# Performance work log

Hardware: AMD Instinct MI355X
Metric: run time of the kernel (lower is better)

Reference implementation:

```python
import jax, jax.numpy as jnp
import numpy as np

V, E, HD, K = 100000, 128, 256, 9
B, T = 128, 512
H = HD // 2  # per-direction hidden size


def setup_inputs() -> dict:
    key = jax.random.key(0)
    ks = jax.random.split(key, 16)
    s = 0.1
    rn = lambda k, shape: jax.random.normal(k, shape, jnp.float32) * s
    sentences = jax.random.randint(ks[0], (B, T), 0, V, dtype=jnp.int32)
    lengths = jax.random.randint(ks[1], (B,), 1, T + 1, dtype=jnp.int32)
    return {
        'sentences': sentences,
        'lengths': lengths,
        'embed': rn(ks[2], (V, E)),
        'Wih_f': rn(ks[3], (4 * H, E)), 'Whh_f': rn(ks[4], (4 * H, H)),
        'bih_f': rn(ks[5], (4 * H,)), 'bhh_f': rn(ks[6], (4 * H,)),
        'Wih_b': rn(ks[7], (4 * H, E)), 'Whh_b': rn(ks[8], (4 * H, H)),
        'bih_b': rn(ks[9], (4 * H,)), 'bhh_b': rn(ks[10], (4 * H,)),
        'W_out': rn(ks[11], (K, HD)), 'b_out': rn(ks[12], (K,)),
        'start_t': rn(ks[13], (K,)), 'end_t': rn(ks[14], (K,)),
        'trans': rn(ks[15], (K, K)),
    }


def _lstm(x, mask, Wih, Whh, bih, bhh, reverse):
    # x: [B,T,E], mask: [B,T] bool. Replicates packed-sequence semantics:
    # state frozen and output zeroed at padding positions (padding is trailing,
    # so reverse=True starts fresh at each sequence's true end).
    Bv, Hv = x.shape[0], Whh.shape[1]
    bias = bih + bhh

    def step(carry, inp):
        h, c = carry
        x_t, m_t = inp  # [B,E], [B,1]
        gates = x_t @ Wih.T + h @ Whh.T + bias  # [B,4H]
        i, f, g, o = jnp.split(gates, 4, axis=-1)  # torch gate order i,f,g,o
        c_new = jax.nn.sigmoid(f) * c + jax.nn.sigmoid(i) * jnp.tanh(g)
        h_new = jax.nn.sigmoid(o) * jnp.tanh(c_new)
        h = jnp.where(m_t, h_new, h)
        c = jnp.where(m_t, c_new, c)
        return (h, c), h * m_t.astype(h.dtype)

    init = (jnp.zeros((Bv, Hv), x.dtype), jnp.zeros((Bv, Hv), x.dtype))
    xs = (jnp.swapaxes(x, 0, 1), jnp.swapaxes(mask, 0, 1)[..., None])
    _, hs = jax.lax.scan(step, init, xs, reverse=reverse)
    return jnp.swapaxes(hs, 0, 1)  # [B,T,H]


def _emissions(sentences, mask, embed, Wih_f, Whh_f, bih_f, bhh_f,
               Wih_b, Whh_b, bih_b, bhh_b, W_out, b_out):
    x = embed[sentences]  # [B,T,E] (dropout is identity at inference)
    hf = _lstm(x, mask, Wih_f, Whh_f, bih_f, bhh_f, reverse=False)
    hb = _lstm(x, mask, Wih_b, Whh_b, bih_b, bhh_b, reverse=True)
    h = jnp.concatenate([hf, hb], axis=-1)  # [B,T,2H]
    return jnp.einsum('btd,kd->btk', h, W_out) + b_out  # [B,T,K]


def _viterbi(em, mask, start_t, end_t, trans):
    # torchcrf-style batched Viterbi decode. em: [B,T,K], mask: [B,T] bool.
    Kv = em.shape[-1]
    ident = jnp.arange(Kv, dtype=jnp.int32)[None]  # identity backpointers for pads
    score0 = start_t[None] + em[:, 0]  # [B,K]

    def step(score, inp):
        em_t, m_t = inp  # [B,K], [B,1]
        cand = score[:, :, None] + trans[None] + em_t[:, None, :]  # [B,K_prev,K_cur]
        new_score = cand.max(axis=1)
        idx = cand.argmax(axis=1).astype(jnp.int32)  # [B,K]
        score = jnp.where(m_t, new_score, score)
        idx = jnp.where(m_t, idx, ident)
        return score, idx

    xs = (jnp.swapaxes(em[:, 1:], 0, 1), jnp.swapaxes(mask[:, 1:], 0, 1)[..., None])
    score, hist = jax.lax.scan(step, score0, xs)  # hist: [T-1,B,K]
    score = score + end_t[None]
    last_tag = jnp.argmax(score, axis=-1).astype(jnp.int32)  # [B]

    def back(tag, idx_t):
        prev = jnp.take_along_axis(idx_t, tag[:, None], axis=1)[:, 0]
        return prev, prev

    _, tags_prev = jax.lax.scan(back, last_tag, hist, reverse=True)  # [T-1,B]
    tags = jnp.swapaxes(jnp.concatenate([tags_prev, last_tag[None]], axis=0), 0, 1)
    return jnp.where(mask, tags, 0), score.max(axis=-1)


def reference(sentences, lengths, embed, Wih_f, Whh_f, bih_f, bhh_f,
              Wih_b, Whh_b, bih_b, bhh_b, W_out, b_out, start_t, end_t, trans):
    mask = jnp.arange(sentences.shape[1])[None] < lengths[:, None]  # [B,T]
    em = _emissions(sentences, mask, embed, Wih_f, Whh_f, bih_f, bhh_f,
                    Wih_b, Whh_b, bih_b, bhh_b, W_out, b_out)
    tags, _ = _viterbi(em, mask, start_t, end_t, trans)
    return tags  # [B,T] int32, padded positions set to 0
```

## Files before the change

kernel.cpp:

```cpp
#include <hip/hip_runtime.h>
#include <cmath>

#define B_  128
#define T_  512
#define E_  128
#define H_  128
#define G4  512
#define K_  9

__global__ __launch_bounds__(256)
void gather_x(const int* __restrict__ sent, const float* __restrict__ embed,
              float* __restrict__ Xt)
{
  const int m = blockIdx.x * 256 + threadIdx.x;
  const int vid = sent[m];
  const float* er = embed + (size_t)vid * E_;
  const size_t MT = (size_t)B_ * T_;
#pragma unroll
  for (int q = 0; q < 32; ++q) {
    float4 v = *(const float4*)(er + q * 4);
    Xt[(size_t)(q * 4 + 0) * MT + m] = v.x;
    Xt[(size_t)(q * 4 + 1) * MT + m] = v.y;
    Xt[(size_t)(q * 4 + 2) * MT + m] = v.z;
    Xt[(size_t)(q * 4 + 3) * MT + m] = v.w;
  }
}

__global__ __launch_bounds__(256)
void transpose_w(const float* __restrict__ Wf, const float* __restrict__ Wb,
                 float* __restrict__ Wt)
{
  const int idx = blockIdx.x * 256 + threadIdx.x;
  const int k = idx >> 10, n = idx & 1023;
  Wt[idx] = (n < 512) ? Wf[n * E_ + k] : Wb[(n - 512) * E_ + k];
}

__global__ __launch_bounds__(256, 2)
void proj_gemm(const float* __restrict__ Xt, const float* __restrict__ Wt,
               const float* __restrict__ bif, const float* __restrict__ bhf,
               const float* __restrict__ bib, const float* __restrict__ bhb,
               float* __restrict__ proj, int t0f, int Tc)
{
  __shared__ __align__(16) float Al[128 * 64];
  __shared__ __align__(16) float Bl[128 * 64];
  const int tid   = threadIdx.x;
  const int ntile = blockIdx.x;
  const int mtile = blockIdx.y;
  const int tpb   = Tc >> 6;
  const int b     = mtile / tpb;
  const int toff  = (mtile - b * tpb) << 6;
  const int dir   = ntile >> 3;
  const int t0    = dir ? (T_ - t0f - Tc) : t0f;
  const int n0    = (ntile & 7) << 6;

  {
    const int r4 = tid & 15;
    const int ks = tid >> 4;
    const size_t MT = (size_t)B_ * T_;
    const int mbase = b * T_ + t0 + toff;
    const int nbase = dir * 512 + n0;
#pragma unroll
    for (int p = 0; p < 8; ++p) {
      const int k = ks * 8 + p;
      float4 a4 = *(const float4*)(Xt + (size_t)k * MT + mbase + r4 * 4);
      float4 b4 = *(const float4*)(Wt + k * 1024 + nbase + r4 * 4);
      *(float4*)&Al[k * 64 + r4 * 4] = a4;
      *(float4*)&Bl[k * 64 + r4 * 4] = b4;
    }
  }
  __syncthreads();

  const int mg = tid & 15, ng = tid >> 4;
  float acc[4][4] = {};
#pragma unroll 8
  for (int k = 0; k < 128; ++k) {
    float4 a  = *(const float4*)&Al[k * 64 + mg * 4];
    float4 bb = *(const float4*)&Bl[k * 64 + ng * 4];
    acc[0][0] += a.x * bb.x; acc[0][1] += a.x * bb.y; acc[0][2] += a.x * bb.z; acc[0][3] += a.x * bb.w;
    acc[1][0] += a.y * bb.x; acc[1][1] += a.y * bb.y; acc[1][2] += a.y * bb.z; acc[1][3] += a.y * bb.w;
    acc[2][0] += a.z * bb.x; acc[2][1] += a.z * bb.y; acc[2][2] += a.z * bb.z; acc[2][3] += a.z * bb.w;
    acc[3][0] += a.w * bb.x; acc[3][1] += a.w * bb.y; acc[3][2] += a.w * bb.z; acc[3][3] += a.w * bb.w;
  }

  const float* bi = dir ? bib : bif;
  const float* bh = dir ? bhb : bhf;
  const int nl = ng * 4;
  float4 bias;
  bias.x = bi[n0 + nl + 0] + bh[n0 + nl + 0];
  bias.y = bi[n0 + nl + 1] + bh[n0 + nl + 1];
  bias.z = bi[n0 + nl + 2] + bh[n0 + nl + 2];
  bias.w = bi[n0 + nl + 3] + bh[n0 + nl + 3];
#pragma unroll
  for (int i = 0; i < 4; ++i) {
    const int tloc = toff + mg * 4 + i;
    float4 o;
    o.x = acc[i][0] + bias.x; o.y = acc[i][1] + bias.y;
    o.z = acc[i][2] + bias.z; o.w = acc[i][3] + bias.w;
    *(float4*)&proj[((size_t)(b * Tc + tloc)) * 1024 + dir * G4 + n0 + nl] = o;
  }
}

__device__ __forceinline__ float fast_rcp(float x) {
  return __builtin_amdgcn_rcpf(x);
}
__device__ __forceinline__ float fast_sig(float x) {
  return fast_rcp(1.f + __expf(-x));
}
__device__ __forceinline__ float fast_tanh(float x) {
  return 2.f * fast_rcp(1.f + __expf(-2.f * x)) - 1.f;
}

__global__ __launch_bounds__(512, 2)
void lstm_chunk(const float* __restrict__ proj,
                const float* __restrict__ Whf, const float* __restrict__ Whb,
                const int* __restrict__ lengths,
                float* __restrict__ hs,
                float* __restrict__ sh, float* __restrict__ sc,
                int t0f, int Tc, int first)
{
  const int dir = blockIdx.x;
  const int b   = blockIdx.y;
  const int tid = threadIdx.x;
  const int l   = tid & 63;
  const int wv  = tid >> 6;
  const int u   = wv * 16 + (l & 15);
  const int gp  = (l >> 4) & 1;
  const int kh  = l >> 5;
  const int rowA = u + (gp ? 256 : 0);
  const int rowB = rowA + 128;
  const float* __restrict__ Whh = dir ? Whb : Whf;
  __shared__ __align__(16) float h_hist[2][H_];

  float wA[64], wB[64];
  {
    const float* wra = Whh + (size_t)rowA * H_ + kh * 64;
    const float* wrb = Whh + (size_t)rowB * H_ + kh * 64;
#pragma unroll
    for (int k = 0; k < 64; k += 4) {
      float4 va = *(const float4*)(wra + k);
      float4 vb = *(const float4*)(wrb + k);
      wA[k] = va.x; wA[k + 1] = va.y; wA[k + 2] = va.z; wA[k + 3] = va.w;
      wB[k] = vb.x; wB[k + 1] = vb.y; wB[k + 2] = vb.z; wB[k + 3] = vb.w;
    }
  }
#pragma unroll
  for (int k = 0; k < 64; ++k) {
    asm volatile("" : "+v"(wA[k]));
    asm volatile("" : "+v"(wB[k]));
  }

  const int len = lengths[b];
  const int t0  = dir ? (T_ - t0f - Tc) : t0f;
  const float fgp = (float)gp;
  const float kf  = 1.f + fgp;
  float c = 0.f, h_reg = 0.f;
  if (!first) {
    c     = sc[(dir * B_ + b) * H_ + u];
    h_reg = sh[(dir * B_ + b) * H_ + u];
  }
  if (l < 16) h_hist[1][u] = h_reg;
  __syncthreads();

  const float* projpA = proj + (size_t)b * Tc * 1024 + dir * G4 + rowA;
  const float* projpB = projpA + 128;
  const int tc00 = dir ? (Tc - 1) : 0;
  float pvA = projpA[(size_t)tc00 * 1024];
  float pvB = projpB[(size_t)tc00 * 1024];

  for (int s = 0; s < Tc; ++s) {
    const int tc = dir ? (Tc - 1 - s) : s;
    const int t  = t0 + tc;
    float nvA = 0.f, nvB = 0.f;
    if (s + 1 < Tc) {
      const int tcn = dir ? (Tc - 2 - s) : (s + 1);
      nvA = projpA[(size_t)tcn * 1024];
      nvB = projpB[(size_t)tcn * 1024];
    }
    const float* hp = h_hist[(s + 1) & 1] + kh * 64;
    float a0 = 0.f, a1 = 0.f, a2 = 0.f, a3 = 0.f;
#pragma unroll
    for (int k4 = 0; k4 < 16; ++k4) {
      float4 h4 = *(const float4*)&hp[k4 * 4];
      a0 += wA[4 * k4 + 0] * h4.x; a1 += wA[4 * k4 + 1] * h4.y;
      a0 += wA[4 * k4 + 2] * h4.z; a1 += wA[4 * k4 + 3] * h4.w;
      a2 += wB[4 * k4 + 0] * h4.x; a3 += wB[4 * k4 + 1] * h4.y;
      a2 += wB[4 * k4 + 2] * h4.z; a3 += wB[4 * k4 + 3] * h4.w;
    }
    float sA = a0 + a1; sA += __shfl_xor(sA, 32); sA += pvA;
    float sB = a2 + a3; sB += __shfl_xor(sB, 32); sB += pvB;
    const float gA = kf * fast_rcp(1.f + __expf(-kf * sA)) - fgp;
    const float gB = fast_sig(sB);
    const float xA = __shfl_xor(gA, 16);
    const float xB = __shfl_xor(gB, 16);
    const float gi = gp ? xA : gA;
    const float gf = gp ? xB : gB;
    const float gg = gp ? gA : xA;
    const float go = gp ? gB : xB;
    const float cn = gf * c + gi * gg;
    const float hn = go * fast_tanh(cn);
    const bool  m  = (t < len);
    c     = m ? cn : c;
    h_reg = m ? hn : h_reg;
    if (l < 16) {
      h_hist[s & 1][u] = h_reg;
      hs[(size_t)(b * T_ + t) * 256 + dir * H_ + u] = m ? hn : 0.f;
    }
    __syncthreads();
    pvA = nvA; pvB = nvB;
  }
  if (l < 16 && wv == (u >> 4)) {
    sh[(dir * B_ + b) * H_ + u] = h_reg;
    sc[(dir * B_ + b) * H_ + u] = c;
  }
}

__global__ __launch_bounds__(256)
void emis_kernel(const float* __restrict__ hs, const float* __restrict__ Wout,
                 const float* __restrict__ bout, float* __restrict__ em)
{
  __shared__ __align__(16) float Wl[K_ * 256];
  const int tid = threadIdx.x;
  for (int i = tid; i < K_ * 256; i += 256) Wl[i] = Wout[i];
  __syncthreads();
  const int m = blockIdx.x * 256 + tid;
  const float* h = hs + (size_t)m * 256;
  float acc[K_] = {};
#pragma unroll 4
  for (int kk = 0; kk < 64; ++kk) {
    float4 h4 = *(const float4*)(h + kk * 4);
#pragma unroll
    for (int k9 = 0; k9 < K_; ++k9) {
      float4 w4 = *(const float4*)&Wl[k9 * 256 + kk * 4];
      acc[k9] += h4.x * w4.x + h4.y * w4.y + h4.z * w4.z + h4.w * w4.w;
    }
  }
#pragma unroll
  for (int k9 = 0; k9 < K_; ++k9) em[(size_t)m * K_ + k9] = acc[k9] + bout[k9];
}

__global__ __launch_bounds__(64)
void viterbi_kernel(const float* __restrict__ em, const int* __restrict__ lengths,
                    const float* __restrict__ st, const float* __restrict__ en,
                    const float* __restrict__ trans, int* __restrict__ tags)
{
  const int b    = blockIdx.x;
  const int lane = threadIdx.x;
  __shared__ unsigned char hist[(T_ - 1) * 16];
  const int len = lengths[b];
  float tr[K_];
#pragma unroll
  for (int j = 0; j < K_; ++j) tr[j] = (lane < K_) ? trans[j * K_ + lane] : 0.f;
  float s = (lane < K_) ? st[lane] + em[(size_t)(b * T_) * K_ + lane] : -1e30f;
  for (int t = 1; t < len; ++t) {
    float best = -1e30f; int bj = 0;
#pragma unroll
    for (int j = 0; j < K_; ++j) {
      float v = __shfl(s, j) + tr[j];
      if (v > best) { best = v; bj = j; }
    }
    if (lane < K_) {
      s = best + em[(size_t)(b * T_ + t) * K_ + lane];
      hist[(t - 1) * 16 + lane] = (unsigned char)bj;
    }
  }
  float fs = (lane < K_) ? s + en[lane] : -1e30f;
  float best = -1e30f; int last = 0;
#pragma unroll
  for (int j = 0; j < K_; ++j) {
    float v = __shfl(fs, j);
    if (v > best) { best = v; last = j; }
  }
  __syncthreads();
  if (lane == 0) {
    int tag = last;
    tags[b * T_ + len - 1] = tag;
    for (int t = len - 2; t >= 0; --t) {
      tag = hist[t * 16 + tag];
      tags[b * T_ + t] = tag;
    }
  }
  for (int t = len + lane; t < T_; t += 64) tags[b * T_ + t] = 0;
}

extern "C" void kernel_launch(void* const* d_in, const int* in_sizes, int n_in,
                              void* d_out, int out_size, void* d_ws, size_t ws_size,
                              hipStream_t stream)
{
  const int*   sent  = (const int*)d_in[0];
  const int*   lens  = (const int*)d_in[1];
  const float* embed = (const float*)d_in[2];
  const float* Wif   = (const float*)d_in[3];
  const float* Whf   = (const float*)d_in[4];
  const float* bif   = (const float*)d_in[5];
  const float* bhf   = (const float*)d_in[6];
  const float* Wib   = (const float*)d_in[7];
  const float* Whb   = (const float*)d_in[8];
  const float* bib   = (const float*)d_in[9];
  const float* bhb   = (const float*)d_in[10];
  const float* Wout  = (const float*)d_in[11];
  const float* bout  = (const float*)d_in[12];
  const float* stt   = (const float*)d_in[13];
  const float* ent   = (const float*)d_in[14];
  const float* trans = (const float*)d_in[15];
  int* tags = (int*)d_out;

  float* ws   = (float*)d_ws;
  float* hs   = ws;
  float* em   = hs + (size_t)B_ * T_ * 256;
  float* sh   = em + (size_t)B_ * T_ * K_;
  float* sc   = sh + (size_t)2 * B_ * H_;
  float* Xt   = sc + (size_t)2 * B_ * H_;
  float* Wt   = Xt + (size_t)E_ * B_ * T_;
  float* proj = Wt + (size_t)E_ * 1024;
  const size_t fixed_bytes = (size_t)(proj - ws) * sizeof(float);

  int Tc = 512;
  while (Tc > 64 && fixed_bytes + (size_t)B_ * Tc * 1024 * sizeof(float) > ws_size)
    Tc >>= 1;

  hipLaunchKernelGGL(gather_x, dim3((B_ * T_) / 256), dim3(256), 0, stream,
                     sent, embed, Xt);
  hipLaunchKernelGGL(transpose_w, dim3((E_ * 1024) / 256), dim3(256), 0, stream,
                     Wif, Wib, Wt);

  const int nch = T_ / Tc;
  for (int c2 = 0; c2 < nch; ++c2) {
    const int t0f = c2 * Tc;
    dim3 g1(16, B_ * (Tc >> 6));
    hipLaunchKernelGGL(proj_gemm, g1, dim3(256), 0, stream,
                       Xt, Wt, bif, bhf, bib, bhb, proj, t0f, Tc);
    dim3 g2(2, B_);
    hipLaunchKernelGGL(lstm_chunk, g2, dim3(512), 0, stream,
                       proj, Whf, Whb, lens, hs, sh, sc, t0f, Tc, (int)(c2 == 0));
  }
  hipLaunchKernelGGL(emis_kernel, dim3((B_ * T_) / 256), dim3(256), 0, stream,
                     hs, Wout, bout, em);
  hipLaunchKernelGGL(viterbi_kernel, dim3(B_), dim3(64), 0, stream,
                     em, lens, stt, ent, trans, tags);
}
```

Before: 850.9 us.

## Enlarge projection GEMM tile to 128x128 with double-buffered K-slices

Rewrites the input-projection GEMM to compute a 128x128 output tile per block, with each thread accumulating 8x8 instead of 4x4, and streams K in 32-wide slices through double-buffered shared memory. Global loads for the next slice are issued into registers before the current slice is computed. The aim is more FLOPs per shared-memory load and overlap of global loads with compute. The costs are higher register pressure (launch_bounds occupancy hint dropped), fewer blocks, and a minimum chunk size of 128 time steps.

```diff
diff --git a/kernel.cpp b/kernel.cpp
--- a/kernel.cpp
+++ b/kernel.cpp
@@ -35,68 +35,111 @@
   Wt[idx] = (n < 512) ? Wf[n * E_ + k] : Wb[(n - 512) * E_ + k];
 }
 
-__global__ __launch_bounds__(256, 2)
+#define MT8(L, R, A)                                                  \
+  L.x += A * B0.x; L.y += A * B0.y; L.z += A * B0.z; L.w += A * B0.w; \
+  R.x += A * B1.x; R.y += A * B1.y; R.z += A * B1.z; R.w += A * B1.w;
+
+__global__ __launch_bounds__(256)
 void proj_gemm(const float* __restrict__ Xt, const float* __restrict__ Wt,
                const float* __restrict__ bif, const float* __restrict__ bhf,
                const float* __restrict__ bib, const float* __restrict__ bhb,
                float* __restrict__ proj, int t0f, int Tc)
 {
-  __shared__ __align__(16) float Al[128 * 64];
-  __shared__ __align__(16) float Bl[128 * 64];
+  __shared__ __align__(16) float Al[2][32][128];
+  __shared__ __align__(16) float Bl[2][32][128];
   const int tid   = threadIdx.x;
   const int ntile = blockIdx.x;
   const int mtile = blockIdx.y;
-  const int tpb   = Tc >> 6;
-  const int b     = mtile / tpb;
-  const int toff  = (mtile - b * tpb) << 6;
-  const int dir   = ntile >> 3;
+  const int dir   = ntile >> 2;
+  const int n0    = (ntile & 3) << 7;
   const int t0    = dir ? (T_ - t0f - Tc) : t0f;
-  const int n0    = (ntile & 7) << 6;
-
-  {
-    const int r4 = tid & 15;
-    const int ks = tid >> 4;
-    const size_t MT = (size_t)B_ * T_;
-    const int mbase = b * T_ + t0 + toff;
-    const int nbase = dir * 512 + n0;
-#pragma unroll
-    for (int p = 0; p < 8; ++p) {
-      const int k = ks * 8 + p;
-      float4 a4 = *(const float4*)(Xt + (size_t)k * MT + mbase + r4 * 4);
-      float4 b4 = *(const float4*)(Wt + k * 1024 + nbase + r4 * 4);
-      *(float4*)&Al[k * 64 + r4 * 4] = a4;
-      *(float4*)&Bl[k * 64 + r4 * 4] = b4;
-    }
+  const int mrow0 = mtile * 128;
+  const int b     = mrow0 / Tc;
+  const size_t MT = (size_t)B_ * T_;
+  const int mbase = b * T_ + t0 + (mrow0 - b * Tc);
+  const int nbase = dir * 512 + n0;
+
+  const int kk0 = tid >> 5;
+  const int mq0 = (tid & 31) * 4;
+
+  float4 pa[4], pb[4];
+#pragma unroll
+  for (int j = 0; j < 4; ++j) {
+    const int kk = kk0 + j * 8;
+    pa[j] = *(const float4*)(Xt + (size_t)kk * MT + mbase + mq0);
+    pb[j] = *(const float4*)(Wt + kk * 1024 + nbase + mq0);
+  }
+#pragma unroll
+  for (int j = 0; j < 4; ++j) {
+    const int kk = kk0 + j * 8;
+    *(float4*)&Al[0][kk][mq0] = pa[j];
+    *(float4*)&Bl[0][kk][mq0] = pb[j];
   }
   __syncthreads();
 
   const int mg = tid & 15, ng = tid >> 4;
-  float acc[4][4] = {};
-#pragma unroll 8
-  for (int k = 0; k < 128; ++k) {
-    float4 a  = *(const float4*)&Al[k * 64 + mg * 4];
-    float4 bb = *(const float4*)&Bl[k * 64 + ng * 4];
-    acc[0][0] += a.x * bb.x; acc[0][1] += a.x * bb.y; acc[0][2] += a.x * bb.z; acc[0][3] += a.x * bb.w;
-    acc[1][0] += a.y * bb.x; acc[1][1] += a.y * bb.y; acc[1][2] += a.y * bb.z; acc[1][3] += a.y * bb.w;
-    acc[2][0] += a.z * bb.x; acc[2][1] += a.z * bb.y; acc[2][2] += a.z * bb.z; acc[2][3] += a.z * bb.w;
-    acc[3][0] += a.w * bb.x; acc[3][1] += a.w * bb.y; acc[3][2] += a.w * bb.z; acc[3][3] += a.w * bb.w;
+  float4 accL[8] = {}, accR[8] = {};
+  for (int s = 0; s < 4; ++s) {
+    if (s < 3) {
+      const int kb = (s + 1) * 32;
+#pragma unroll
+      for (int j = 0; j < 4; ++j) {
+        const int kk = kb + kk0 + j * 8;
+        pa[j] = *(const float4*)(Xt + (size_t)kk * MT + mbase + mq0);
+        pb[j] = *(const float4*)(Wt + kk * 1024 + nbase + mq0);
+      }
+    }
+    const int bs = s & 1;
+#pragma unroll
+    for (int k = 0; k < 32; ++k) {
+      float4 A0 = *(const float4*)&Al[bs][k][mg * 4];
+      float4 A1 = *(const float4*)&Al[bs][k][64 + mg * 4];
+      float4 B0 = *(const float4*)&Bl[bs][k][ng * 4];
+      float4 B1 = *(const float4*)&Bl[bs][k][64 + ng * 4];
+      MT8(accL[0], accR[0], A0.x)
+      MT8(accL[1], accR[1], A0.y)
+      MT8(accL[2], accR[2], A0.z)
+      MT8(accL[3], accR[3], A0.w)
+      MT8(accL[4], accR[4], A1.x)
+      MT8(accL[5], accR[5], A1.y)
+      MT8(accL[6], accR[6], A1.z)
+      MT8(accL[7], accR[7], A1.w)
+    }
+    if (s < 3) {
+      __syncthreads();
+      const int nb = bs ^ 1;
+#pragma unroll
+      for (int j = 0; j < 4; ++j) {
+        const int kk = kk0 + j * 8;
+        *(float4*)&Al[nb][kk][mq0] = pa[j];
+        *(float4*)&Bl[nb][kk][mq0] = pb[j];
+      }
+      __syncthreads();
+    }
   }
 
   const float* bi = dir ? bib : bif;
   const float* bh = dir ? bhb : bhf;
-  const int nl = ng * 4;
-  float4 bias;
-  bias.x = bi[n0 + nl + 0] + bh[n0 + nl + 0];
-  bias.y = bi[n0 + nl + 1] + bh[n0 + nl + 1];
-  bias.z = bi[n0 + nl + 2] + bh[n0 + nl + 2];
-  bias.w = bi[n0 + nl + 3] + bh[n0 + nl + 3];
-#pragma unroll
-  for (int i = 0; i < 4; ++i) {
-    const int tloc = toff + mg * 4 + i;
-    float4 o;
-    o.x = acc[i][0] + bias.x; o.y = acc[i][1] + bias.y;
-    o.z = acc[i][2] + bias.z; o.w = acc[i][3] + bias.w;
-    *(float4*)&proj[((size_t)(b * Tc + tloc)) * 1024 + dir * G4 + n0 + nl] = o;
+  float4 biasL, biasR;
+  biasL.x = bi[n0 + ng * 4 + 0] + bh[n0 + ng * 4 + 0];
+  biasL.y = bi[n0 + ng * 4 + 1] + bh[n0 + ng * 4 + 1];
+  biasL.z = bi[n0 + ng * 4 + 2] + bh[n0 + ng * 4 + 2];
+  biasL.w = bi[n0 + ng * 4 + 3] + bh[n0 + ng * 4 + 3];
+  biasR.x = bi[n0 + 64 + ng * 4 + 0] + bh[n0 + 64 + ng * 4 + 0];
+  biasR.y = bi[n0 + 64 + ng * 4 + 1] + bh[n0 + 64 + ng * 4 + 1];
+  biasR.z = bi[n0 + 64 + ng * 4 + 2] + bh[n0 + 64 + ng * 4 + 2];
+  biasR.w = bi[n0 + 64 + ng * 4 + 3] + bh[n0 + 64 + ng * 4 + 3];
+#pragma unroll
+  for (int i = 0; i < 8; ++i) {
+    const int mrow = mrow0 + (i >> 2) * 64 + mg * 4 + (i & 3);
+    float* prow = proj + (size_t)mrow * 1024 + dir * G4 + n0;
+    float4 oL, oR;
+    oL.x = accL[i].x + biasL.x; oL.y = accL[i].y + biasL.y;
+    oL.z = accL[i].z + biasL.z; oL.w = accL[i].w + biasL.w;
+    oR.x = accR[i].x + biasR.x; oR.y = accR[i].y + biasR.y;
+    oR.z = accR[i].z + biasR.z; oR.w = accR[i].w + biasR.w;
+    *(float4*)&prow[ng * 4]      = oL;
+    *(float4*)&prow[64 + ng * 4] = oR;
   }
 }
 
@@ -315,7 +358,7 @@
   const size_t fixed_bytes = (size_t)(proj - ws) * sizeof(float);
 
   int Tc = 512;
-  while (Tc > 64 && fixed_bytes + (size_t)B_ * Tc * 1024 * sizeof(float) > ws_size)
+  while (Tc > 128 && fixed_bytes + (size_t)B_ * Tc * 1024 * sizeof(float) > ws_size)
     Tc >>= 1;
 
   hipLaunchKernelGGL(gather_x, dim3((B_ * T_) / 256), dim3(256), 0, stream,
@@ -326,7 +369,7 @@
   const int nch = T_ / Tc;
   for (int c2 = 0; c2 < nch; ++c2) {
     const int t0f = c2 * Tc;
-    dim3 g1(16, B_ * (Tc >> 6));
+    dim3 g1(8, (B_ * Tc) >> 7);
     hipLaunchKernelGGL(proj_gemm, g1, dim3(256), 0, stream,
                        Xt, Wt, bif, bhf, bib, bhb, proj, t0f, Tc);
     dim3 g2(2, B_);
```

Result: slower. 1.536 ms (+80.5%).
